# Optimization experiments

Hardware: AMD Instinct MI355X
Metric: run time of the kernel (lower is better)

## Reference

```python
import jax, jax.numpy as jnp
import numpy as np

EMBED_DIM = 1024
NUM_HEADS = 16
HEAD_DIM = EMBED_DIM // NUM_HEADS
SEG_LENS = [1024, 2048, 4096]
DIL_RATIOS = [1, 2, 4]
NEG = -1e8  # lse fill value used by sparse_to_dense


def setup_inputs() -> dict:
    root = jax.random.key(0)
    ks = jax.random.split(root, 12)
    B, L, E = 1, 4096, EMBED_DIM
    s = 0.02
    return {
        "query": jax.random.normal(ks[0], (B, L, E), jnp.float32),
        "key": jax.random.normal(ks[1], (B, L, E), jnp.float32),
        "value": jax.random.normal(ks[2], (B, L, E), jnp.float32),
        "Wq": jax.random.normal(ks[3], (E, E), jnp.float32) * s,
        "bq": jnp.zeros((E,), jnp.float32),
        "Wk": jax.random.normal(ks[4], (E, E), jnp.float32) * s,
        "bk": jnp.zeros((E,), jnp.float32),
        "Wv": jax.random.normal(ks[5], (E, E), jnp.float32) * s,
        "bv": jnp.zeros((E,), jnp.float32),
        "Wo": jax.random.normal(ks[6], (E, E), jnp.float32) * s,
        "bo": jnp.zeros((E,), jnp.float32),
    }


def _branch(q, k, v, sl, dr, L):
    """One (segment_length, dilated_ratio) branch.
    q,k,v: (B, L, H, D). Returns dense out (B, H, L, D) and lse (B, H, L).
    """
    B = q.shape[0]
    H, D = NUM_HEADS, HEAD_DIM
    sl = min(sl, L)
    pad = (-L) % sl
    if pad:
        pw = ((0, 0), (0, pad), (0, 0), (0, 0))
        q, k, v = jnp.pad(q, pw), jnp.pad(k, pw), jnp.pad(v, pw)
    n = (L + pad) // sl  # segments
    qs = q.reshape(B * n, sl, H, D)
    ks = k.reshape(B * n, sl, H, D)
    vs = v.reshape(B * n, sl, H, D)
    # dense_to_sparse: head j (group r = j // (H//dr)) keeps positions i*dr + r
    hg = H // dr
    g = sl // dr
    grp = jnp.arange(H) // hg                      # (H,)
    pos = jnp.arange(g)[:, None] * dr + grp[None]  # (g, H) dense positions
    hidx = jnp.arange(H)[None, :]
    sp = lambda x: x[:, pos, hidx, :]              # (B*n, g, H, D)
    qd, kd, vd = sp(qs), sp(ks), sp(vs)
    # causal attention within each sparse segment (flash_attn semantics)
    scores = jnp.einsum('bqhd,bkhd->bhqk', qd, kd) * (D ** -0.5)
    mask = jnp.tril(jnp.ones((g, g), bool))
    scores = jnp.where(mask, scores, -jnp.inf)
    lse = jax.nn.logsumexp(scores, axis=-1)        # (B*n, H, g)
    o = jnp.einsum('bhqk,bkhd->bqhd', jnp.exp(scores - lse[..., None]), vd)
    # sparse_to_dense: scatter back onto dense positions, NEG elsewhere
    hcol = jnp.arange(H)[:, None]                  # (H,1)
    od = jnp.zeros((B * n, H, sl, D), o.dtype).at[:, hcol, pos.T].set(
        o.transpose(0, 2, 1, 3))
    ld = jnp.zeros((B * n, H, sl), lse.dtype).at[:, hcol, pos.T].set(lse)
    ld = jnp.where(ld == 0.0, NEG, ld)  # matches masked_fill_(lse == 0, -1e8)
    od = od.reshape(B, n, H, sl, D).transpose(0, 2, 1, 3, 4)
    od = od.reshape(B, H, n * sl, D)[:, :, :L]
    ld = ld.reshape(B, n, H, sl).transpose(0, 2, 1, 3).reshape(B, H, n * sl)[:, :, :L]
    return od, ld


def reference(query, key, value, Wq, bq, Wk, bk, Wv, bv, Wo, bo):
    B, L, E = query.shape
    H, D = NUM_HEADS, HEAD_DIM
    q = (query @ Wq.T + bq).reshape(B, L, H, D)
    k = (key @ Wk.T + bk).reshape(B, L, H, D)
    v = (value @ Wv.T + bv).reshape(B, L, H, D)
    outs, lses = [], []
    for sl, dr in zip(SEG_LENS, DIL_RATIOS):
        o, l = _branch(q, k, v, sl, dr, L)
        outs.append(o)
        lses.append(l)
    lse_all = jnp.stack(lses, 0)[..., None]        # (nb, B, H, L, 1)
    m = lse_all.max(0)
    w = jnp.exp(lse_all - m)
    w = w / w.sum(0)                               # softmax merge weights
    w = jax.lax.stop_gradient(w)                   # torch computes under no_grad
    out = sum(o * wi.astype(o.dtype) for o, wi in zip(outs, w))  # (B,H,L,D)
    out = out.transpose(0, 2, 1, 3).reshape(B, L, E)
    return out @ Wo.T + bo
```

## Files before the change

kernel.cpp:

```cpp
#include <hip/hip_runtime.h>
#include <math.h>


#define L_SEQ 4096
#define EDIM  1024
#define NH    16
#define HD    64
#define GLEN  1024

typedef __bf16 bf16;
typedef __bf16 bf16x8 __attribute__((ext_vector_type(8)));
typedef __bf16 bf16x4 __attribute__((ext_vector_type(4)));
typedef short  s16x4  __attribute__((ext_vector_type(4)));
typedef float  f32x4  __attribute__((ext_vector_type(4)));

__device__ __forceinline__ void gload16(const bf16* g, bf16* l) {
  __builtin_amdgcn_global_load_lds(
      (__attribute__((address_space(1))) void*)(const_cast<bf16*>(g)),
      (__attribute__((address_space(3))) void*)(l),
      16, 0, 0);
}

__device__ __forceinline__ f32x4 mfma16x16x16_bf16(bf16x4 a, bf16x4 b, f32x4 c) {
#if defined(__HIP_DEVICE_COMPILE__)
  union { bf16x4 h; s16x4 s; } ua, ub;
  ua.h = a; ub.h = b;
  return __builtin_amdgcn_mfma_f32_16x16x16bf16_1k(ua.s, ub.s, c, 0, 0, 0);
#else
  (void)a; (void)b;
  return c;
#endif
}

__device__ __forceinline__ float fast_exp2(float x) {
#if __has_builtin(__builtin_amdgcn_exp2f)
  return __builtin_amdgcn_exp2f(x);
#else
  return __expf(x * 0.6931471805599453f);
#endif
}

__global__ __launch_bounds__(256) void cvt_kernel(
    const float* q, const float* k, const float* v,
    const float* wq, const float* wk, const float* wv, const float* wo,
    bf16* oq, bf16* ok, bf16* ov,
    bf16* owq, bf16* owk, bf16* owv, bf16* owo)
{
  const float* src; bf16* dst; int n;
  switch (blockIdx.y) {
    case 0: src = q;  dst = oq;  n = L_SEQ*EDIM; break;
    case 1: src = k;  dst = ok;  n = L_SEQ*EDIM; break;
    case 2: src = v;  dst = ov;  n = L_SEQ*EDIM; break;
    case 3: src = wq; dst = owq; n = EDIM*EDIM; break;
    case 4: src = wk; dst = owk; n = EDIM*EDIM; break;
    case 5: src = wv; dst = owv; n = EDIM*EDIM; break;
    default: src = wo; dst = owo; n = EDIM*EDIM; break;
  }
  int i = (blockIdx.x * 256 + threadIdx.x) * 8;
  if (i >= n) return;
  const float4* s4 = (const float4*)(src + i);
  float4 a = s4[0], b = s4[1];
  bf16x8 o = { (bf16)a.x, (bf16)a.y, (bf16)a.z, (bf16)a.w,
               (bf16)b.x, (bf16)b.y, (bf16)b.z, (bf16)b.w };
  *(bf16x8*)(dst + i) = o;
}

template <typename OutT>
__device__ __forceinline__ void gemm_body(const bf16* __restrict__ A,
                                          const bf16* __restrict__ W,
                                          const float* __restrict__ bias,
                                          OutT* __restrict__ C)
{
  constexpr int K = 1024;
  __shared__ __align__(16) bf16 lA[128 * 32];
  __shared__ __align__(16) bf16 lB[128 * 32];

  const int tid  = threadIdx.x;
  const int lane = tid & 63;
  const int w    = tid >> 6;
  const int quad = lane >> 4;
  const int l16  = lane & 15;
  const int wr   = w >> 1, wc = w & 1;
  const int row0 = blockIdx.y * 128;
  const int col0 = blockIdx.x * 128;

  f32x4 acc[4][4] = {};

  const int c0 = tid, c1 = tid + 256;
  const bf16* Ab0 = A + (size_t)(row0 + (c0 >> 2)) * K + (c0 & 3) * 8;
  const bf16* Ab1 = A + (size_t)(row0 + (c1 >> 2)) * K + (c1 & 3) * 8;
  const bf16* Bb0 = W + (size_t)(col0 + (c0 >> 2)) * K + (c0 & 3) * 8;
  const bf16* Bb1 = W + (size_t)(col0 + (c1 >> 2)) * K + (c1 & 3) * 8;
  bf16* lA0 = &lA[c0 * 8]; bf16* lA1 = &lA[c1 * 8];
  bf16* lB0 = &lB[c0 * 8]; bf16* lB1 = &lB[c1 * 8];

  for (int kt = 0; kt < K; kt += 32) {
    __syncthreads();
    gload16(Ab0 + kt, lA0);
    gload16(Ab1 + kt, lA1);
    gload16(Bb0 + kt, lB0);
    gload16(Bb1 + kt, lB1);
    __syncthreads();

    bf16x8 af[4], bfrag[4];
#pragma unroll
    for (int mi = 0; mi < 4; mi++)
      af[mi] = *(const bf16x8*)&lA[(wr * 64 + mi * 16 + l16) * 32 + quad * 8];
#pragma unroll
    for (int ni = 0; ni < 4; ni++)
      bfrag[ni] = *(const bf16x8*)&lB[(wc * 64 + ni * 16 + l16) * 32 + quad * 8];
#pragma unroll
    for (int mi = 0; mi < 4; mi++)
#pragma unroll
      for (int ni = 0; ni < 4; ni++)
        acc[mi][ni] = __builtin_amdgcn_mfma_f32_16x16x32_bf16(
            af[mi], bfrag[ni], acc[mi][ni], 0, 0, 0);
  }

#pragma unroll
  for (int mi = 0; mi < 4; mi++) {
#pragma unroll
    for (int ni = 0; ni < 4; ni++) {
      const int gcol = col0 + wc * 64 + ni * 16 + l16;
      const float bv = bias[gcol];
#pragma unroll
      for (int r = 0; r < 4; r++) {
        const int grow = row0 + wr * 64 + mi * 16 + quad * 4 + r;
        C[(size_t)grow * 1024 + gcol] = (OutT)(acc[mi][ni][r] + bv);
      }
    }
  }
}

__global__ __launch_bounds__(256) void gemm_qkv_kernel(
    const bf16* xq, const bf16* xk, const bf16* xv,
    const bf16* wq, const bf16* wk, const bf16* wv,
    const float* bq, const float* bk, const float* bv,
    bf16* q, bf16* k, bf16* v)
{
  const bf16 *A, *W; const float* bias; bf16* C;
  if (blockIdx.z == 0)      { A = xq; W = wq; bias = bq; C = q; }
  else if (blockIdx.z == 1) { A = xk; W = wk; bias = bk; C = k; }
  else                      { A = xv; W = wv; bias = bv; C = v; }
  gemm_body<bf16>(A, W, bias, C);
}

__global__ __launch_bounds__(256) void gemm_out_kernel(
    const bf16* A, const bf16* W, const float* bias, float* C)
{
  gemm_body<float>(A, W, bias, C);
}

__global__ __launch_bounds__(256) void vtrans_kernel(
    const bf16* __restrict__ v, bf16* vt0, bf16* vt1, bf16* vt2)
{
  __shared__ __align__(16) bf16 ltile[64 * 72];
  const int bid = blockIdx.x;
  int sl, dr, rem, shift; bf16* vt;
  if (bid < 1024)      { sl = 1024; dr = 1; rem = bid;        vt = vt0; shift = 4; }
  else if (bid < 1536) { sl = 2048; dr = 2; rem = bid - 1024; vt = vt1; shift = 3; }
  else                 { sl = 4096; dr = 4; rem = bid - 1536; vt = vt2; shift = 2; }
  const int ktile = rem & 15;
  const int h     = (rem >> 4) & 15;
  const int seg   = rem >> 8;
  const int grp   = h >> shift;
  const int segbase = seg * sl;
  const int tid = threadIdx.x;
  {
    const int i = tid >> 2, dc = tid & 3;
    const size_t p = (size_t)(segbase + (ktile * 64 + i) * dr + grp);
    const bf16* src = v + p * EDIM + h * 64 + dc * 16;
    *(uint4*)&ltile[i * 72 + dc * 16]     = *(const uint4*)(src);
    *(uint4*)&ltile[i * 72 + dc * 16 + 8] = *(const uint4*)(src + 8);
  }
  __syncthreads();
  {
    const int d = tid >> 2, kc = tid & 3;
    __align__(16) bf16 tmp[16];
#pragma unroll
    for (int j = 0; j < 16; j++) tmp[j] = ltile[(kc * 16 + j) * 72 + d];
    bf16* dst = vt + ((size_t)(seg * NH + h) * 64 + d) * GLEN + ktile * 64 + kc * 16;
    *(uint4*)dst       = *(uint4*)&tmp[0];
    *(uint4*)(dst + 8) = *(uint4*)&tmp[8];
  }
}

__global__ __launch_bounds__(256, 4) void attn_kernel(
    const bf16* __restrict__ qg, const bf16* __restrict__ kg,
    const bf16* vt0, const bf16* vt1, const bf16* vt2,
    bf16* o0, bf16* o1, bf16* o2,
    float* l0, float* l1, float* l2)
{
  __shared__ __align__(16) bf16 lK[2][64 * 64];
  __shared__ __align__(16) bf16 lV[2][64 * 64];

  const int bid0 = blockIdx.x;
  const int o = (bid0 & 7) * 112 + (bid0 >> 3);

  int sl, dr, rem, shift;
  const bf16* vt; bf16* ob; float* lseb;
  if (o < 512)      { sl = 1024; dr = 1; rem = o;       vt = vt0; ob = o0; lseb = l0; shift = 4; }
  else if (o < 768) { sl = 2048; dr = 2; rem = o - 512; vt = vt1; ob = o1; lseb = l1; shift = 3; }
  else              { sl = 4096; dr = 4; rem = o - 768; vt = vt2; ob = o2; lseb = l2; shift = 2; }
  const int j   = rem & 7;
  const int h   = (rem >> 3) & 15;
  const int seg = rem >> 7;
  const int qtA = 15 - j;
  const int qtB = j;
  const int grp = h >> shift;
  const int segbase = seg * sl;

  const int tid = threadIdx.x, lane = tid & 63, w = tid >> 6;
  const int quad = lane >> 4, l16 = lane & 15;

  auto loadq = [&](int qt, bf16x8& a0, bf16x8& a1) {
    const int qi = qt * 64 + w * 16 + l16;
    const size_t p = (size_t)(segbase + qi * dr + grp);
    const bf16* qp = qg + p * EDIM + h * 64 + quad * 8;
    a0 = *(const bf16x8*)(qp);
    a1 = *(const bf16x8*)(qp + 32);
  };
  bf16x8 qaA0, qaA1, qaB0, qaB1;
  loadq(qtA, qaA0, qaA1);
  loadq(qtB, qaB0, qaB1);

  f32x4 OA[4] = {}, OB[4] = {};
  float mA = -__builtin_inff(), lAcc = 0.f;
  float mB = -__builtin_inff(), lBcc = 0.f;

  const bf16* vbase = vt + (size_t)(seg * NH + h) * 64 * GLEN;
  const int c0 = tid, c1 = tid + 256;
  const int r0 = c0 >> 3, sw0 = ((c0 & 7) ^ (r0 & 7));
  const int r1 = c1 >> 3, sw1 = ((c1 & 7) ^ (r1 & 7));

  auto stage = [&](int kt, int buf) {
    const bf16* kp0 = kg + (size_t)(segbase + (kt * 64 + r0) * dr + grp) * EDIM + h * 64 + sw0 * 8;
    const bf16* kp1 = kg + (size_t)(segbase + (kt * 64 + r1) * dr + grp) * EDIM + h * 64 + sw1 * 8;
    gload16(kp0, &lK[buf][c0 * 8]);
    gload16(kp1, &lK[buf][c1 * 8]);
    const bf16* vp0 = vbase + (size_t)r0 * GLEN + kt * 64 + sw0 * 8;
    const bf16* vp1 = vbase + (size_t)r1 * GLEN + kt * 64 + sw1 * 8;
    gload16(vp0, &lV[buf][c0 * 8]);
    gload16(vp1, &lV[buf][c1 * 8]);
  };

  const float CS = 0.18033688011112042f;

  auto tile_compute = [&](const bf16* bK, const bf16* bV,
                          const bf16x8& qa0, const bf16x8& qa1,
                          f32x4 (&Oa)[4], float& m_r, float& l_r,
                          const bool diag, const int kt, const int qi_lane) {
    const int tmax = diag ? w : 3;

    f32x4 s[4];
#pragma unroll
    for (int t = 0; t < 4; t++) {
      if (t <= tmax) {
        s[t] = f32x4{0.f, 0.f, 0.f, 0.f};
        const int kj = t * 16 + l16;
        const int rs = kj & 7;
        bf16x8 ka0 = *(const bf16x8*)&bK[kj * 64 + ((quad       ^ rs) * 8)];
        bf16x8 ka1 = *(const bf16x8*)&bK[kj * 64 + (((4 + quad) ^ rs) * 8)];
        s[t] = __builtin_amdgcn_mfma_f32_16x16x32_bf16(ka0, qa0, s[t], 0, 0, 0);
        s[t] = __builtin_amdgcn_mfma_f32_16x16x32_bf16(ka1, qa1, s[t], 0, 0, 0);
      }
    }

    float mraw = -__builtin_inff();
#pragma unroll
    for (int t = 0; t < 4; t++) {
      if (t <= tmax) {
#pragma unroll
        for (int r = 0; r < 4; r++) {
          float sv = s[t][r];
          if (diag) {
            const int kj = kt * 64 + t * 16 + quad * 4 + r;
            if (kj > qi_lane) sv = -__builtin_inff();
          }
          s[t][r] = sv;
          mraw = fmaxf(mraw, sv);
        }
      }
    }
    mraw = fmaxf(mraw, __shfl_xor(mraw, 16, 64));
    mraw = fmaxf(mraw, __shfl_xor(mraw, 32, 64));
    const float mloc = mraw * CS;
    const float mnew = fmaxf(m_r, mloc);
    if (mnew - m_r > 8.0f) {
      const float alpha = fast_exp2(m_r - mnew);
#pragma unroll
      for (int nf = 0; nf < 4; nf++)
#pragma unroll
        for (int r = 0; r < 4; r++) Oa[nf][r] *= alpha;
      l_r *= alpha;
      m_r = mnew;
    }

    bf16x4 pb[4];
    float rs_sum = 0.f;
#pragma unroll
    for (int t = 0; t < 4; t++) {
      if (t <= tmax) {
#pragma unroll
        for (int r = 0; r < 4; r++) {
          const float pv = fast_exp2(__builtin_fmaf(s[t][r], CS, -m_r));
          pb[t][r] = (bf16)pv;
          rs_sum += pv;
        }
      }
    }
    rs_sum += __shfl_xor(rs_sum, 16, 64);
    rs_sum += __shfl_xor(rs_sum, 32, 64);
    l_r += rs_sum;

#pragma unroll
    for (int t = 0; t < 4; t++) {
      if (t <= tmax) {
        const int ck  = 2 * t + (quad >> 1);
        const int sub = (quad & 1) * 4;
#pragma unroll
        for (int nf = 0; nf < 4; nf++) {
          const int drow = nf * 16 + l16;
          bf16x4 va = *(const bf16x4*)&bV[drow * 64 + ((ck ^ (drow & 7)) * 8) + sub];
          Oa[nf] = mfma16x16x16_bf16(va, pb[t], Oa[nf]);
        }
      }
    }
  };

  const int qiA = qtA * 64 + w * 16 + l16;
  const int qiB = qtB * 64 + w * 16 + l16;

  stage(0, 0);
  for (int kt = 0; kt <= qtA; kt++) {
    __syncthreads();
    if (kt < qtA) stage(kt + 1, (kt + 1) & 1);
    const bf16* bK = lK[kt & 1];
    const bf16* bV = lV[kt & 1];
    tile_compute(bK, bV, qaA0, qaA1, OA, mA, lAcc, kt == qtA, kt, qiA);
    if (kt <= qtB)
      tile_compute(bK, bV, qaB0, qaB1, OB, mB, lBcc, kt == qtB, kt, qiB);
  }

  auto epilogue = [&](const f32x4 (&Oa)[4], float m_r, float l_r, int qt) {
    const int qi = qt * 64 + w * 16 + l16;
    const float linv = 1.0f / l_r;
    const int pdense = segbase + qi * dr + grp;
    bf16* orow = ob + (size_t)pdense * EDIM + h * 64;
#pragma unroll
    for (int nf = 0; nf < 4; nf++) {
      bf16x4 ov;
#pragma unroll
      for (int r = 0; r < 4; r++) ov[r] = (bf16)(Oa[nf][r] * linv);
      *(bf16x4*)(orow + nf * 16 + quad * 4) = ov;
    }
    if (quad == 0)
      lseb[h * L_SEQ + pdense] = m_r * 0.6931471805599453f + __logf(l_r);
  };
  epilogue(OA, mA, lAcc, qtA);
  epilogue(OB, mB, lBcc, qtB);
}

__global__ __launch_bounds__(256) void merge_kernel(
    const bf16* __restrict__ o0, const bf16* __restrict__ o1, const bf16* __restrict__ o2,
    const float* __restrict__ l0, const float* __restrict__ l1, const float* __restrict__ l2,
    bf16* __restrict__ merged)
{
  const int idx = blockIdx.x * 256 + threadIdx.x;
  const int dc = idx & 7;
  const int h  = (idx >> 3) & 15;
  const int p  = idx >> 7;
  const bool c1 = ((p & 1) == (h >> 3));
  const bool c2 = ((p & 3) == (h >> 2));
  const float s0 = l0[h * L_SEQ + p];
  const float s1 = c1 ? l1[h * L_SEQ + p] : -__builtin_inff();
  const float s2 = c2 ? l2[h * L_SEQ + p] : -__builtin_inff();
  const float mx = fmaxf(s0, fmaxf(s1, s2));
  float w0 = __expf(s0 - mx);
  float w1 = c1 ? __expf(s1 - mx) : 0.f;
  float w2 = c2 ? __expf(s2 - mx) : 0.f;
  const float inv = 1.0f / (w0 + w1 + w2);
  w0 *= inv; w1 *= inv; w2 *= inv;

  const size_t off = (size_t)p * EDIM + h * 64 + dc * 8;
  float acc[8];
  bf16x8 a0 = *(const bf16x8*)(o0 + off);
#pragma unroll
  for (int j = 0; j < 8; j++) acc[j] = w0 * (float)a0[j];
  if (c1) {
    bf16x8 a1 = *(const bf16x8*)(o1 + off);
#pragma unroll
    for (int j = 0; j < 8; j++) acc[j] += w1 * (float)a1[j];
  }
  if (c2) {
    bf16x8 a2 = *(const bf16x8*)(o2 + off);
#pragma unroll
    for (int j = 0; j < 8; j++) acc[j] += w2 * (float)a2[j];
  }
  bf16x8 r;
#pragma unroll
  for (int j = 0; j < 8; j++) r[j] = (bf16)acc[j];
  *(bf16x8*)(merged + off) = r;
}

extern "C" void kernel_launch(void* const* d_in, const int* in_sizes, int n_in,
                              void* d_out, int out_size, void* d_ws, size_t ws_size,
                              hipStream_t stream)
{
  (void)in_sizes; (void)n_in; (void)out_size; (void)ws_size;
  const float* query = (const float*)d_in[0];
  const float* key   = (const float*)d_in[1];
  const float* value = (const float*)d_in[2];
  const float* Wq = (const float*)d_in[3];
  const float* bq = (const float*)d_in[4];
  const float* Wk = (const float*)d_in[5];
  const float* bk = (const float*)d_in[6];
  const float* Wv = (const float*)d_in[7];
  const float* bv = (const float*)d_in[8];
  const float* Wo = (const float*)d_in[9];
  const float* bo = (const float*)d_in[10];

  char* base = (char*)d_ws;
  size_t off = 0;
  auto take = [&](size_t nbytes) -> char* {
    char* p = base + off;
    off += (nbytes + 255) & ~(size_t)255;
    return p;
  };
  const size_t LE2 = (size_t)L_SEQ * EDIM * 2;
  const size_t EE2 = (size_t)EDIM * EDIM * 2;
  bf16* xq  = (bf16*)take(LE2);
  bf16* xk  = (bf16*)take(LE2);
  bf16* xv  = (bf16*)take(LE2);
  bf16* wqb = (bf16*)take(EE2);
  bf16* wkb = (bf16*)take(EE2);
  bf16* wvb = (bf16*)take(EE2);
  bf16* wob = (bf16*)take(EE2);
  bf16* qb  = (bf16*)take(LE2);
  bf16* kb  = (bf16*)take(LE2);
  bf16* vb  = (bf16*)take(LE2);
  bf16* vt0 = (bf16*)take((size_t)4 * NH * HD * GLEN * 2);
  bf16* vt1 = (bf16*)take((size_t)2 * NH * HD * GLEN * 2);
  bf16* vt2 = (bf16*)take((size_t)1 * NH * HD * GLEN * 2);
  float* lse0 = (float*)take((size_t)NH * L_SEQ * 4);
  float* lse1 = (float*)take((size_t)NH * L_SEQ * 4);
  float* lse2 = (float*)take((size_t)NH * L_SEQ * 4);
  bf16* merged = (bf16*)take(LE2);
  bf16* o0 = xq; bf16* o1 = xk; bf16* o2 = xv;

  dim3 blk(256);
  cvt_kernel<<<dim3(2048, 7), blk, 0, stream>>>(
      query, key, value, Wq, Wk, Wv, Wo, xq, xk, xv, wqb, wkb, wvb, wob);
  gemm_qkv_kernel<<<dim3(8, 32, 3), blk, 0, stream>>>(
      xq, xk, xv, wqb, wkb, wvb, bq, bk, bv, qb, kb, vb);
  vtrans_kernel<<<dim3(1792), blk, 0, stream>>>(vb, vt0, vt1, vt2);
  attn_kernel<<<dim3(896), blk, 0, stream>>>(
      qb, kb, vt0, vt1, vt2, o0, o1, o2, lse0, lse1, lse2);
  merge_kernel<<<dim3(2048), blk, 0, stream>>>(
      o0, o1, o2, lse0, lse1, lse2, merged);
  gemm_out_kernel<<<dim3(8, 32), blk, 0, stream>>>(merged, wob, bo, (float*)d_out);
}
```

Before: 249.6 us.

## Fuse both query tiles' attention compute to share K/V LDS reads

Merges the two per-block query tiles (A and B) into one compute routine, so each K and V fragment read from LDS feeds the MFMAs of both tiles. The key loop is split into three phases, with compile-time flags for whether tile B is active and which tile is on its diagonal, which removes runtime masking branches. Global-load addresses now advance by pointer increments instead of being recomputed each step, and the online-softmax rescale test becomes wave-uniform via __all. In exchange, more accumulators are live at once, which raises register pressure and could reduce occupancy.

After: 228.8 us. -8.4%, faster.

```diff
diff --git a/kernel.cpp b/kernel.cpp
--- a/kernel.cpp
+++ b/kernel.cpp
@@ -13,6 +13,8 @@
 typedef __bf16 bf16x4 __attribute__((ext_vector_type(4)));
 typedef short  s16x4  __attribute__((ext_vector_type(4)));
 typedef float  f32x4  __attribute__((ext_vector_type(4)));
+
+template <bool B> struct Flag { static constexpr bool v = B; };
 
 __device__ __forceinline__ void gload16(const bf16* g, bf16* l) {
   __builtin_amdgcn_global_load_lds(
@@ -212,6 +214,7 @@
 
   const int tid = threadIdx.x, lane = tid & 63, w = tid >> 6;
   const int quad = lane >> 4, l16 = lane & 15;
+  const int rs8 = l16 & 7;
 
   auto loadq = [&](int qt, bf16x8& a0, bf16x8& a1) {
     const int qi = qt * 64 + w * 16 + l16;
@@ -225,122 +228,188 @@
   loadq(qtB, qaB0, qaB1);
 
   f32x4 OA[4] = {}, OB[4] = {};
-  float mA = -__builtin_inff(), lAcc = 0.f;
-  float mB = -__builtin_inff(), lBcc = 0.f;
+  float mA = -__builtin_inff(), lA_ = 0.f;
+  float mB = -__builtin_inff(), lB_ = 0.f;
 
   const bf16* vbase = vt + (size_t)(seg * NH + h) * 64 * GLEN;
   const int c0 = tid, c1 = tid + 256;
   const int r0 = c0 >> 3, sw0 = ((c0 & 7) ^ (r0 & 7));
   const int r1 = c1 >> 3, sw1 = ((c1 & 7) ^ (r1 & 7));
 
-  auto stage = [&](int kt, int buf) {
-    const bf16* kp0 = kg + (size_t)(segbase + (kt * 64 + r0) * dr + grp) * EDIM + h * 64 + sw0 * 8;
-    const bf16* kp1 = kg + (size_t)(segbase + (kt * 64 + r1) * dr + grp) * EDIM + h * 64 + sw1 * 8;
+  const bf16* kp0 = kg + (size_t)(segbase + r0 * dr + grp) * EDIM + h * 64 + sw0 * 8;
+  const bf16* kp1 = kg + (size_t)(segbase + r1 * dr + grp) * EDIM + h * 64 + sw1 * 8;
+  const bf16* vp0 = vbase + (size_t)r0 * GLEN + sw0 * 8;
+  const bf16* vp1 = vbase + (size_t)r1 * GLEN + sw1 * 8;
+  const size_t kstep = (size_t)64 * dr * EDIM;
+
+  auto stage = [&](int buf) {
     gload16(kp0, &lK[buf][c0 * 8]);
     gload16(kp1, &lK[buf][c1 * 8]);
-    const bf16* vp0 = vbase + (size_t)r0 * GLEN + kt * 64 + sw0 * 8;
-    const bf16* vp1 = vbase + (size_t)r1 * GLEN + kt * 64 + sw1 * 8;
     gload16(vp0, &lV[buf][c0 * 8]);
     gload16(vp1, &lV[buf][c1 * 8]);
+    kp0 += kstep; kp1 += kstep; vp0 += 64; vp1 += 64;
   };
 
   const float CS = 0.18033688011112042f;
-
-  auto tile_compute = [&](const bf16* bK, const bf16* bV,
-                          const bf16x8& qa0, const bf16x8& qa1,
-                          f32x4 (&Oa)[4], float& m_r, float& l_r,
-                          const bool diag, const int kt, const int qi_lane) {
-    const int tmax = diag ? w : 3;
-
-    f32x4 s[4];
-#pragma unroll
-    for (int t = 0; t < 4; t++) {
-      if (t <= tmax) {
-        s[t] = f32x4{0.f, 0.f, 0.f, 0.f};
-        const int kj = t * 16 + l16;
-        const int rs = kj & 7;
-        bf16x8 ka0 = *(const bf16x8*)&bK[kj * 64 + ((quad       ^ rs) * 8)];
-        bf16x8 ka1 = *(const bf16x8*)&bK[kj * 64 + (((4 + quad) ^ rs) * 8)];
-        s[t] = __builtin_amdgcn_mfma_f32_16x16x32_bf16(ka0, qa0, s[t], 0, 0, 0);
-        s[t] = __builtin_amdgcn_mfma_f32_16x16x32_bf16(ka1, qa1, s[t], 0, 0, 0);
-      }
-    }
-
-    float mraw = -__builtin_inff();
-#pragma unroll
-    for (int t = 0; t < 4; t++) {
-      if (t <= tmax) {
-#pragma unroll
-        for (int r = 0; r < 4; r++) {
-          float sv = s[t][r];
-          if (diag) {
-            const int kj = kt * 64 + t * 16 + quad * 4 + r;
-            if (kj > qi_lane) sv = -__builtin_inff();
-          }
-          s[t][r] = sv;
-          mraw = fmaxf(mraw, sv);
-        }
-      }
-    }
-    mraw = fmaxf(mraw, __shfl_xor(mraw, 16, 64));
-    mraw = fmaxf(mraw, __shfl_xor(mraw, 32, 64));
-    const float mloc = mraw * CS;
-    const float mnew = fmaxf(m_r, mloc);
-    if (mnew - m_r > 8.0f) {
-      const float alpha = fast_exp2(m_r - mnew);
-#pragma unroll
-      for (int nf = 0; nf < 4; nf++)
-#pragma unroll
-        for (int r = 0; r < 4; r++) Oa[nf][r] *= alpha;
-      l_r *= alpha;
-      m_r = mnew;
-    }
-
-    bf16x4 pb[4];
-    float rs_sum = 0.f;
-#pragma unroll
-    for (int t = 0; t < 4; t++) {
-      if (t <= tmax) {
-#pragma unroll
-        for (int r = 0; r < 4; r++) {
-          const float pv = fast_exp2(__builtin_fmaf(s[t][r], CS, -m_r));
-          pb[t][r] = (bf16)pv;
-          rs_sum += pv;
-        }
-      }
-    }
-    rs_sum += __shfl_xor(rs_sum, 16, 64);
-    rs_sum += __shfl_xor(rs_sum, 32, 64);
-    l_r += rs_sum;
-
-#pragma unroll
-    for (int t = 0; t < 4; t++) {
-      if (t <= tmax) {
-        const int ck  = 2 * t + (quad >> 1);
-        const int sub = (quad & 1) * 4;
-#pragma unroll
-        for (int nf = 0; nf < 4; nf++) {
-          const int drow = nf * 16 + l16;
-          bf16x4 va = *(const bf16x4*)&bV[drow * 64 + ((ck ^ (drow & 7)) * 8) + sub];
-          Oa[nf] = mfma16x16x16_bf16(va, pb[t], Oa[nf]);
-        }
-      }
-    }
-  };
-
   const int qiA = qtA * 64 + w * 16 + l16;
   const int qiB = qtB * 64 + w * 16 + l16;
 
-  stage(0, 0);
-  for (int kt = 0; kt <= qtA; kt++) {
-    __syncthreads();
-    if (kt < qtA) stage(kt + 1, (kt + 1) & 1);
+  const int kb0 = l16 * 64 + ((quad ^ rs8) * 8);
+  const int kb1 = l16 * 64 + (((4 + quad) ^ rs8) * 8);
+  const int vb0 = l16 * 64 + (quad & 1) * 4;
+
+  auto comp = [&](auto hasB_, auto diagA_, auto diagB_, int kt) {
+    constexpr bool HAS_B  = decltype(hasB_)::v;
+    constexpr bool DIAG_A = decltype(diagA_)::v;
+    constexpr bool DIAG_B = decltype(diagB_)::v;
     const bf16* bK = lK[kt & 1];
     const bf16* bV = lV[kt & 1];
-    tile_compute(bK, bV, qaA0, qaA1, OA, mA, lAcc, kt == qtA, kt, qiA);
-    if (kt <= qtB)
-      tile_compute(bK, bV, qaB0, qaB1, OB, mB, lBcc, kt == qtB, kt, qiB);
-  }
+
+    f32x4 sA[4], sB[4];
+#pragma unroll
+    for (int t = 0; t < 4; t++) {
+      const bool aA = !DIAG_A || t <= w;
+      const bool aB = HAS_B && (!DIAG_B || t <= w);
+      if (aA || aB) {
+        bf16x8 ka0 = *(const bf16x8*)&bK[kb0 + t * 1024];
+        bf16x8 ka1 = *(const bf16x8*)&bK[kb1 + t * 1024];
+        if (aA) {
+          sA[t] = f32x4{0.f, 0.f, 0.f, 0.f};
+          sA[t] = __builtin_amdgcn_mfma_f32_16x16x32_bf16(ka0, qaA0, sA[t], 0, 0, 0);
+          sA[t] = __builtin_amdgcn_mfma_f32_16x16x32_bf16(ka1, qaA1, sA[t], 0, 0, 0);
+        }
+        if (aB) {
+          sB[t] = f32x4{0.f, 0.f, 0.f, 0.f};
+          sB[t] = __builtin_amdgcn_mfma_f32_16x16x32_bf16(ka0, qaB0, sB[t], 0, 0, 0);
+          sB[t] = __builtin_amdgcn_mfma_f32_16x16x32_bf16(ka1, qaB1, sB[t], 0, 0, 0);
+        }
+      }
+    }
+
+    float mrA = -__builtin_inff(), mrB = -__builtin_inff();
+#pragma unroll
+    for (int t = 0; t < 4; t++) {
+      if (!DIAG_A || t <= w) {
+#pragma unroll
+        for (int r = 0; r < 4; r++) {
+          float sv = sA[t][r];
+          if (DIAG_A) {
+            const int kj = kt * 64 + t * 16 + quad * 4 + r;
+            if (kj > qiA) sv = -__builtin_inff();
+          }
+          sA[t][r] = sv;
+          mrA = fmaxf(mrA, sv);
+        }
+      }
+      if (HAS_B && (!DIAG_B || t <= w)) {
+#pragma unroll
+        for (int r = 0; r < 4; r++) {
+          float sv = sB[t][r];
+          if (DIAG_B) {
+            const int kj = kt * 64 + t * 16 + quad * 4 + r;
+            if (kj > qiB) sv = -__builtin_inff();
+          }
+          sB[t][r] = sv;
+          mrB = fmaxf(mrB, sv);
+        }
+      }
+    }
+    mrA = fmaxf(mrA, __shfl_xor(mrA, 16, 64));
+    mrA = fmaxf(mrA, __shfl_xor(mrA, 32, 64));
+    if constexpr (HAS_B) {
+      mrB = fmaxf(mrB, __shfl_xor(mrB, 16, 64));
+      mrB = fmaxf(mrB, __shfl_xor(mrB, 32, 64));
+    }
+
+    {
+      const float mnew = fmaxf(mA, mrA * CS);
+      if (!__all(mnew - mA <= 8.0f)) {
+        const float alpha = fast_exp2(mA - mnew);
+#pragma unroll
+        for (int nf = 0; nf < 4; nf++)
+#pragma unroll
+          for (int r = 0; r < 4; r++) OA[nf][r] *= alpha;
+        lA_ *= alpha;
+        mA = mnew;
+      }
+    }
+    if constexpr (HAS_B) {
+      const float mnew = fmaxf(mB, mrB * CS);
+      if (!__all(mnew - mB <= 8.0f)) {
+        const float alpha = fast_exp2(mB - mnew);
+#pragma unroll
+        for (int nf = 0; nf < 4; nf++)
+#pragma unroll
+          for (int r = 0; r < 4; r++) OB[nf][r] *= alpha;
+        lB_ *= alpha;
+        mB = mnew;
+      }
+    }
+
+    bf16x4 pbA[4], pbB[4];
+    float rsA = 0.f, rsB = 0.f;
+#pragma unroll
+    for (int t = 0; t < 4; t++) {
+      if (!DIAG_A || t <= w) {
+#pragma unroll
+        for (int r = 0; r < 4; r++) {
+          const float pv = fast_exp2(__builtin_fmaf(sA[t][r], CS, -mA));
+          pbA[t][r] = (bf16)pv;
+          rsA += pv;
+        }
+      }
+      if (HAS_B && (!DIAG_B || t <= w)) {
+#pragma unroll
+        for (int r = 0; r < 4; r++) {
+          const float pv = fast_exp2(__builtin_fmaf(sB[t][r], CS, -mB));
+          pbB[t][r] = (bf16)pv;
+          rsB += pv;
+        }
+      }
+    }
+    rsA += __shfl_xor(rsA, 16, 64);
+    rsA += __shfl_xor(rsA, 32, 64);
+    lA_ += rsA;
+    if constexpr (HAS_B) {
+      rsB += __shfl_xor(rsB, 16, 64);
+      rsB += __shfl_xor(rsB, 32, 64);
+      lB_ += rsB;
+    }
+
+#pragma unroll
+    for (int t = 0; t < 4; t++) {
+      const bool aA = !DIAG_A || t <= w;
+      const bool aB = HAS_B && (!DIAG_B || t <= w);
+      if (aA || aB) {
+        const int cx = (((2 * t) + (quad >> 1)) ^ rs8) * 8;
+#pragma unroll
+        for (int nf = 0; nf < 4; nf++) {
+          bf16x4 va = *(const bf16x4*)&bV[vb0 + nf * 1024 + cx];
+          if (aA) OA[nf] = mfma16x16x16_bf16(va, pbA[t], OA[nf]);
+          if (aB) OB[nf] = mfma16x16x16_bf16(va, pbB[t], OB[nf]);
+        }
+      }
+    }
+  };
+
+  stage(0);
+  int kt = 0;
+  for (; kt < qtB; kt++) {
+    __syncthreads();
+    stage((kt + 1) & 1);
+    comp(Flag<true>{}, Flag<false>{}, Flag<false>{}, kt);
+  }
+  __syncthreads();
+  stage((kt + 1) & 1);
+  comp(Flag<true>{}, Flag<false>{}, Flag<true>{}, kt);
+  kt++;
+  for (; kt < qtA; kt++) {
+    __syncthreads();
+    stage((kt + 1) & 1);
+    comp(Flag<false>{}, Flag<false>{}, Flag<false>{}, kt);
+  }
+  __syncthreads();
+  comp(Flag<false>{}, Flag<true>{}, Flag<false>{}, kt);
 
   auto epilogue = [&](const f32x4 (&Oa)[4], float m_r, float l_r, int qt) {
     const int qi = qt * 64 + w * 16 + l16;
@@ -357,8 +426,8 @@
     if (quad == 0)
       lseb[h * L_SEQ + pdense] = m_r * 0.6931471805599453f + __logf(l_r);
   };
-  epilogue(OA, mA, lAcc, qtA);
-  epilogue(OB, mB, lBcc, qtB);
+  epilogue(OA, mA, lA_, qtA);
+  epilogue(OB, mB, lB_, qtB);
 }
 
 __global__ __launch_bounds__(256) void merge_kernel(
```
